# Kernel optimization log

Measured on AMD Instinct MI355X. Metric: run time of the kernel, lower is better.

The kernel has to match this reference:

```python
import jax, jax.numpy as jnp
import numpy as np

N_HEADS = 4
N_HIDDEN = 64  # out_features // n_heads
NEG_SLOPE = 0.2


def setup_inputs() -> dict:
    key = jax.random.key(0)
    k1, k2, k3, k4, k5 = jax.random.split(key, 5)
    B, N, F_IN, F_OUT = 1, 4096, 128, 256
    h = jax.random.normal(k1, (B, N, F_IN), dtype=jnp.float32)
    adj_mat = jax.random.uniform(k2, (N, N, 1), dtype=jnp.float32)
    W_proj = jax.random.normal(k3, (F_IN, N_HEADS * N_HIDDEN), dtype=jnp.float32) / np.sqrt(F_IN)
    W_proj_attn = jax.random.normal(k4, (F_IN, N_HEADS * N_HIDDEN // 2), dtype=jnp.float32) / np.sqrt(F_IN)
    w_attn = jax.random.normal(k5, (N_HIDDEN,), dtype=jnp.float32) / np.sqrt(N_HIDDEN)
    return {"h": h, "adj_mat": adj_mat, "W_proj": W_proj, "W_proj_attn": W_proj_attn, "w_attn": w_attn}


def reference(h, adj_mat, W_proj, W_proj_attn, w_attn):
    B, N, _ = h.shape
    H, D = N_HEADS, N_HIDDEN
    half = D // 2
    # value projection: (B, N, H, D)
    g = (h @ W_proj).reshape(B, N, H, D)
    # attention-feature projection: (B, N, H, D//2)
    ga = (h @ W_proj_attn).reshape(B, N, H, half)
    # attn(cat([ga_i, ga_j])) decomposes linearly: e_ij = <w_l, ga_i> + <w_r, ga_j>
    # (identical math to the torch repeat/cat/Linear, without the NxNxD tensor)
    el = jnp.einsum('bnhk,k->bnh', ga, w_attn[:half])   # dest node i term
    er = jnp.einsum('bnhk,k->bnh', ga, w_attn[half:])   # source node j term
    e = jax.nn.leaky_relu(el[:, :, None, :] + er[:, None, :, :], NEG_SLOPE)  # (B, N, N, H)
    mask = adj_mat >= 0.5  # (N, N, 1) broadcasts over (B, N, N, H)
    e = jnp.where(mask, e, -jnp.inf)
    a = jax.nn.softmax(e, axis=2)  # softmax over source nodes j
    # dropout is identity in eval mode
    out = jnp.einsum('bijh,bjhf->bihf', a, g)  # (B, N, H, D)
    return out.reshape(B, N, H * D)  # is_concat=True
```

## Files before the change

### kernel.cpp

```cpp
#include <hip/hip_runtime.h>
#include <hip/hip_bf16.h>

typedef __bf16 bf16_t;
typedef __bf16 bf16x4 __attribute__((ext_vector_type(4)));
typedef __bf16 bf16x8 __attribute__((ext_vector_type(8)));
typedef float floatx4 __attribute__((ext_vector_type(4)));

#define N_NODES 4096
#define F_IN 128
#define NUM_HEADS 4
#define D_HID 64
#define F_OUT 256
#define NEG_SLOPE 0.2f

__global__ __launch_bounds__(384) void proj_kernel(
    const float* __restrict__ hmat, const float* __restrict__ Wp,
    const float* __restrict__ Wa, const float* __restrict__ wattn,
    bf16_t* __restrict__ GB, float* __restrict__ el, float* __restrict__ er)
{
    __shared__ float hl[4][F_IN];
    const int t = threadIdx.x;
    const int j0 = blockIdx.x * 4;

    if (t < 128) {
        const int jl = t >> 5, m0 = (t & 31) * 4;
        *reinterpret_cast<float4*>(&hl[jl][m0]) =
            *reinterpret_cast<const float4*>(&hmat[(size_t)(j0 + jl) * F_IN + m0]);
    }
    __syncthreads();

    float acc[4] = {0.f, 0.f, 0.f, 0.f};

    const float* wptr;
    int stride;
    if (t < 256) { wptr = Wp + t;         stride = 256; }
    else         { wptr = Wa + (t - 256); stride = 128; }

    for (int m = 0; m < F_IN; m += 4) {
        const float w0 = wptr[(size_t)(m + 0) * stride];
        const float w1 = wptr[(size_t)(m + 1) * stride];
        const float w2 = wptr[(size_t)(m + 2) * stride];
        const float w3 = wptr[(size_t)(m + 3) * stride];
#pragma unroll
        for (int jl = 0; jl < 4; ++jl) {
            const float4 hv = *reinterpret_cast<const float4*>(&hl[jl][m]);
            acc[jl] = fmaf(hv.w, w3, fmaf(hv.z, w2, fmaf(hv.y, w1, fmaf(hv.x, w0, acc[jl]))));
        }
    }

    if (t < 256) {
        const int h = t >> 6, f = t & 63;
        bf16x4 o;
#pragma unroll
        for (int q = 0; q < 4; ++q) o[q] = (bf16_t)acc[q];
        const size_t base = ((((size_t)h * 128 + (j0 >> 5)) * 4 + (f >> 4)) * 64
                             + (f & 15) + 16 * ((j0 >> 3) & 3)) * 8 + (j0 & 7);
        *reinterpret_cast<bf16x4*>(&GB[base]) = o;
    } else {
        const int ta = t - 256;
        const int ha = ta >> 5, k = ta & 31;
        const float wl = wattn[k], wr = wattn[32 + k];
#pragma unroll
        for (int jl = 0; jl < 4; ++jl) {
            float vl = acc[jl] * wl;
            float vr = acc[jl] * wr;
#pragma unroll
            for (int s = 16; s >= 1; s >>= 1) {
                vl += __shfl_xor(vl, s, 64);
                vr += __shfl_xor(vr, s, 64);
            }
            if (k == 0) {
                el[ha * N_NODES + j0 + jl] = vl;
                er[ha * N_NODES + j0 + jl] = vr;
            }
        }
    }
}

__global__ __launch_bounds__(1024) void attn_kernel(
    const float* __restrict__ adj, const bf16_t* __restrict__ GB,
    const float* __restrict__ el, const float* __restrict__ er,
    float* __restrict__ numout, float* __restrict__ den_g,
    int njc, int ntiles)
{
    __shared__ bf16_t P_s[NUM_HEADS * 64 * 64];
    __shared__ bf16_t GB_s[32 * 512];

    const int tid = threadIdx.x;
    const int i0  = blockIdx.x * 64;
    const int jc  = blockIdx.y;
    const int jT0 = jc * ntiles * 64;

    const int pi   = tid >> 4;
    const int pj4  = (tid & 15) << 2;
    const int glog = pj4 >> 3;
    const int goff = pj4 & 7;
    const int psw  = ((glog ^ (pi & 7)) << 3) + goff;

    const int wave = tid >> 6;
    const int hh   = wave >> 2;
    const int mt   = wave & 3;
    const int lane = tid & 63;
    const int m    = lane & 15;
    const int quad = lane >> 4;

    float elr[NUM_HEADS];
#pragma unroll
    for (int h = 0; h < NUM_HEADS; ++h) elr[h] = el[h * N_NODES + i0 + pi];

    const float* adjp = adj + (size_t)(i0 + pi) * N_NODES + pj4;

    const int s0 = wave * 2, s1 = s0 + 1;
    const int s0h = (s0 >> 2) & 3, s0f = s0 & 3, s0j = s0 >> 4;
    const int s1h = (s1 >> 2) & 3, s1f = s1 & 3, s1j = s1 >> 4;

    floatx4 acc0 = {0.f, 0.f, 0.f, 0.f};
    floatx4 acc1 = acc0, acc2 = acc0, acc3 = acc0, accd = acc0;
    bf16x8 ones;
#pragma unroll
    for (int q = 0; q < 8; ++q) ones[q] = (bf16_t)1.0f;

    int jb32 = jT0 >> 5;
    float4 adjv = *reinterpret_cast<const float4*>(adjp + jT0);
    float4 gbv0 = *reinterpret_cast<const float4*>(GB + ((size_t)(s0h * 128 + jb32 + s0j) * 4 + s0f) * 512 + lane * 8);
    float4 gbv1 = *reinterpret_cast<const float4*>(GB + ((size_t)(s1h * 128 + jb32 + s1j) * 4 + s1f) * 512 + lane * 8);

    for (int k = 0; k < ntiles; ++k) {
        const int jT = jT0 + k * 64;
        *reinterpret_cast<float4*>(&GB_s[s0 * 512 + lane * 8]) = gbv0;
        *reinterpret_cast<float4*>(&GB_s[s1 * 512 + lane * 8]) = gbv1;
        float4 adjn, gbn0, gbn1;
        if (k + 1 < ntiles) {
            const int jbn = (jT + 64) >> 5;
            adjn = *reinterpret_cast<const float4*>(adjp + jT + 64);
            gbn0 = *reinterpret_cast<const float4*>(GB + ((size_t)(s0h * 128 + jbn + s0j) * 4 + s0f) * 512 + lane * 8);
            gbn1 = *reinterpret_cast<const float4*>(GB + ((size_t)(s1h * 128 + jbn + s1j) * 4 + s1f) * 512 + lane * 8);
        }
        const bool k0 = adjv.x >= 0.5f, k1 = adjv.y >= 0.5f,
                   k2 = adjv.z >= 0.5f, k3 = adjv.w >= 0.5f;
#pragma unroll
        for (int h = 0; h < NUM_HEADS; ++h) {
            const float4 ev = *reinterpret_cast<const float4*>(er + h * N_NODES + jT + pj4);
            float e0 = elr[h] + ev.x, e1 = elr[h] + ev.y,
                  e2 = elr[h] + ev.z, e3 = elr[h] + ev.w;
            e0 = fmaxf(e0, NEG_SLOPE * e0);
            e1 = fmaxf(e1, NEG_SLOPE * e1);
            e2 = fmaxf(e2, NEG_SLOPE * e2);
            e3 = fmaxf(e3, NEG_SLOPE * e3);
            bf16x4 pv;
            pv[0] = (bf16_t)(k0 ? __expf(e0) : 0.f);
            pv[1] = (bf16_t)(k1 ? __expf(e1) : 0.f);
            pv[2] = (bf16_t)(k2 ? __expf(e2) : 0.f);
            pv[3] = (bf16_t)(k3 ? __expf(e3) : 0.f);
            *reinterpret_cast<bf16x4*>(&P_s[(h * 64 + pi) * 64 + psw]) = pv;
        }
        __syncthreads();
#pragma unroll
        for (int kt = 0; kt < 2; ++kt) {
            const int gphys = (((kt * 4 + quad) ^ (m & 7)) << 3);
            const bf16x8 af = *reinterpret_cast<const bf16x8*>(
                &P_s[(hh * 64 + mt * 16 + m) * 64 + gphys]);
            accd = __builtin_amdgcn_mfma_f32_16x16x32_bf16(af, ones, accd, 0, 0, 0);
            const int bb = (kt * 16 + hh * 4) * 512 + lane * 8;
            const bf16x8 b0 = *reinterpret_cast<const bf16x8*>(&GB_s[bb]);
            const bf16x8 b1 = *reinterpret_cast<const bf16x8*>(&GB_s[bb + 512]);
            const bf16x8 b2 = *reinterpret_cast<const bf16x8*>(&GB_s[bb + 1024]);
            const bf16x8 b3 = *reinterpret_cast<const bf16x8*>(&GB_s[bb + 1536]);
            acc0 = __builtin_amdgcn_mfma_f32_16x16x32_bf16(af, b0, acc0, 0, 0, 0);
            acc1 = __builtin_amdgcn_mfma_f32_16x16x32_bf16(af, b1, acc1, 0, 0, 0);
            acc2 = __builtin_amdgcn_mfma_f32_16x16x32_bf16(af, b2, acc2, 0, 0, 0);
            acc3 = __builtin_amdgcn_mfma_f32_16x16x32_bf16(af, b3, acc3, 0, 0, 0);
        }
        if (k + 1 < ntiles) { adjv = adjn; gbv0 = gbn0; gbv1 = gbn1; }
        __syncthreads();
    }

    const int ibase = i0 + mt * 16 + quad * 4;
    if (njc == 1) {
#pragma unroll
        for (int r = 0; r < 4; ++r) {
            const float rd = 1.0f / accd[r];
            float* dst = numout + (size_t)(ibase + r) * F_OUT + hh * D_HID + m;
            dst[0]  = acc0[r] * rd;
            dst[16] = acc1[r] * rd;
            dst[32] = acc2[r] * rd;
            dst[48] = acc3[r] * rd;
        }
    } else {
        float* nrow = numout + (size_t)jc * ((size_t)N_NODES * F_OUT);
#pragma unroll
        for (int r = 0; r < 4; ++r) {
            float* dst = nrow + (size_t)(ibase + r) * F_OUT + hh * D_HID + m;
            dst[0]  = acc0[r];
            dst[16] = acc1[r];
            dst[32] = acc2[r];
            dst[48] = acc3[r];
        }
        if (m == 0) {
#pragma unroll
            for (int r = 0; r < 4; ++r)
                den_g[((size_t)jc * N_NODES + ibase + r) * NUM_HEADS + hh] = accd[r];
        }
    }
}

__global__ __launch_bounds__(256) void reduce_kernel(
    const float* __restrict__ num, const float* __restrict__ den,
    float* __restrict__ out, int njc)
{
    const int idx = blockIdx.x * 256 + threadIdx.x;
    const int i  = idx >> 8;
    const int c  = idx & 255;
    const int hh = c >> 6;
    float n = 0.f, d = 0.f;
    for (int jc = 0; jc < njc; ++jc) {
        n += num[(size_t)jc * ((size_t)N_NODES * F_OUT) + idx];
        d += den[((size_t)jc * N_NODES + i) * NUM_HEADS + hh];
    }
    out[idx] = n / d;
}

extern "C" void kernel_launch(void* const* d_in, const int* in_sizes, int n_in,
                              void* d_out, int out_size, void* d_ws, size_t ws_size,
                              hipStream_t stream)
{
    const float* hmat = (const float*)d_in[0];
    const float* adj  = (const float*)d_in[1];
    const float* Wp   = (const float*)d_in[2];
    const float* Wa   = (const float*)d_in[3];
    const float* watt = (const float*)d_in[4];
    float* out = (float*)d_out;

    char* ws = (char*)d_ws;
    bf16_t* GB = (bf16_t*)ws;
    float*  el = (float*)(ws + (2ull << 20));
    float*  er = (float*)(ws + (2ull << 20) + (64ull << 10));
    const size_t baseoff = (2ull << 20) + (128ull << 10);

    const size_t num_bytes = (size_t)N_NODES * F_OUT * 4;
    const size_t den_bytes = (size_t)N_NODES * NUM_HEADS * 4;
    const int njc = (ws_size >= baseoff + 4 * (num_bytes + den_bytes)) ? 4 : 2;

    float* num = (float*)(ws + baseoff);
    float* den = (float*)(ws + baseoff + (size_t)njc * num_bytes);

    proj_kernel<<<1024, 384, 0, stream>>>(hmat, Wp, Wa, watt, GB, el, er);
    attn_kernel<<<dim3(64, njc), 1024, 0, stream>>>(adj, GB, el, er, num, den,
                                                    njc, (N_NODES / njc) / 64);
    reduce_kernel<<<(N_NODES * F_OUT) / 256, 256, 0, stream>>>(num, den, out, njc);
}
```

Baseline: 156.1 us.

## Factor exp of leaky-relu into precomputed per-node exponentials and halve row tile

Rewrites exp(leaky_relu(el_i+er_j)) as a selected product of per-node exponentials: exp(er) and exp(0.2*er) are precomputed in the projection kernel, exp(el) and exp(0.2*el) per row, and the branch is chosen by comparing against exp(-el). This removes the per-element transcendental from the attention inner loop, replacing it with a compare, a multiply and an extra global load. The attention block is also shrunk to 32 rows and 512 threads, doubling the grid, with each wave staging four GB slices instead of two. Risks are overflow or precision loss in the unnormalized exponent products and a doubled total read of adj-independent GB tiles.

```diff
diff --git a/kernel.cpp b/kernel.cpp
--- a/kernel.cpp
+++ b/kernel.cpp
@@ -16,7 +16,8 @@
 __global__ __launch_bounds__(384) void proj_kernel(
     const float* __restrict__ hmat, const float* __restrict__ Wp,
     const float* __restrict__ Wa, const float* __restrict__ wattn,
-    bf16_t* __restrict__ GB, float* __restrict__ el, float* __restrict__ er)
+    bf16_t* __restrict__ GB, float* __restrict__ el,
+    float* __restrict__ E1r, float* __restrict__ E2r)
 {
     __shared__ float hl[4][F_IN];
     const int t = threadIdx.x;
@@ -70,24 +71,26 @@
                 vr += __shfl_xor(vr, s, 64);
             }
             if (k == 0) {
-                el[ha * N_NODES + j0 + jl] = vl;
-                er[ha * N_NODES + j0 + jl] = vr;
+                el[ha * N_NODES + j0 + jl]  = vl;
+                E1r[ha * N_NODES + j0 + jl] = __expf(vr);
+                E2r[ha * N_NODES + j0 + jl] = __expf(NEG_SLOPE * vr);
             }
         }
     }
 }
 
-__global__ __launch_bounds__(1024) void attn_kernel(
+__global__ __launch_bounds__(512) void attn_kernel(
     const float* __restrict__ adj, const bf16_t* __restrict__ GB,
-    const float* __restrict__ el, const float* __restrict__ er,
+    const float* __restrict__ el, const float* __restrict__ E1r,
+    const float* __restrict__ E2r,
     float* __restrict__ numout, float* __restrict__ den_g,
     int njc, int ntiles)
 {
-    __shared__ bf16_t P_s[NUM_HEADS * 64 * 64];
+    __shared__ bf16_t P_s[NUM_HEADS * 32 * 64];
     __shared__ bf16_t GB_s[32 * 512];
 
     const int tid = threadIdx.x;
-    const int i0  = blockIdx.x * 64;
+    const int i0  = blockIdx.x * 32;
     const int jc  = blockIdx.y;
     const int jT0 = jc * ntiles * 64;
 
@@ -98,21 +101,29 @@
     const int psw  = ((glog ^ (pi & 7)) << 3) + goff;
 
     const int wave = tid >> 6;
-    const int hh   = wave >> 2;
-    const int mt   = wave & 3;
+    const int hh   = wave >> 1;
+    const int mt   = wave & 1;
     const int lane = tid & 63;
     const int m    = lane & 15;
     const int quad = lane >> 4;
 
-    float elr[NUM_HEADS];
-#pragma unroll
-    for (int h = 0; h < NUM_HEADS; ++h) elr[h] = el[h * N_NODES + i0 + pi];
+    float E1i[NUM_HEADS], E2i[NUM_HEADS], Ti[NUM_HEADS];
+#pragma unroll
+    for (int h = 0; h < NUM_HEADS; ++h) {
+        const float e = el[h * N_NODES + i0 + pi];
+        E1i[h] = __expf(e);
+        E2i[h] = __expf(NEG_SLOPE * e);
+        Ti[h]  = __expf(-e);
+    }
 
     const float* adjp = adj + (size_t)(i0 + pi) * N_NODES + pj4;
 
-    const int s0 = wave * 2, s1 = s0 + 1;
-    const int s0h = (s0 >> 2) & 3, s0f = s0 & 3, s0j = s0 >> 4;
-    const int s1h = (s1 >> 2) & 3, s1f = s1 & 3, s1j = s1 >> 4;
+    int sh[4], sf[4], sj[4];
+#pragma unroll
+    for (int ss = 0; ss < 4; ++ss) {
+        const int s = wave * 4 + ss;
+        sh[ss] = (s >> 2) & 3; sf[ss] = s & 3; sj[ss] = s >> 4;
+    }
 
     floatx4 acc0 = {0.f, 0.f, 0.f, 0.f};
     floatx4 acc1 = acc0, acc2 = acc0, acc3 = acc0, accd = acc0;
@@ -120,46 +131,53 @@
 #pragma unroll
     for (int q = 0; q < 8; ++q) ones[q] = (bf16_t)1.0f;
 
-    int jb32 = jT0 >> 5;
+    const int jb32 = jT0 >> 5;
     float4 adjv = *reinterpret_cast<const float4*>(adjp + jT0);
-    float4 gbv0 = *reinterpret_cast<const float4*>(GB + ((size_t)(s0h * 128 + jb32 + s0j) * 4 + s0f) * 512 + lane * 8);
-    float4 gbv1 = *reinterpret_cast<const float4*>(GB + ((size_t)(s1h * 128 + jb32 + s1j) * 4 + s1f) * 512 + lane * 8);
+    float4 gbv[4];
+#pragma unroll
+    for (int ss = 0; ss < 4; ++ss)
+        gbv[ss] = *reinterpret_cast<const float4*>(
+            GB + ((size_t)(sh[ss] * 128 + jb32 + sj[ss]) * 4 + sf[ss]) * 512 + lane * 8);
 
     for (int k = 0; k < ntiles; ++k) {
         const int jT = jT0 + k * 64;
-        *reinterpret_cast<float4*>(&GB_s[s0 * 512 + lane * 8]) = gbv0;
-        *reinterpret_cast<float4*>(&GB_s[s1 * 512 + lane * 8]) = gbv1;
-        float4 adjn, gbn0, gbn1;
+#pragma unroll
+        for (int ss = 0; ss < 4; ++ss)
+            *reinterpret_cast<float4*>(&GB_s[(wave * 4 + ss) * 512 + lane * 8]) = gbv[ss];
+
+        float4 adjn, gbn[4];
         if (k + 1 < ntiles) {
             const int jbn = (jT + 64) >> 5;
             adjn = *reinterpret_cast<const float4*>(adjp + jT + 64);
-            gbn0 = *reinterpret_cast<const float4*>(GB + ((size_t)(s0h * 128 + jbn + s0j) * 4 + s0f) * 512 + lane * 8);
-            gbn1 = *reinterpret_cast<const float4*>(GB + ((size_t)(s1h * 128 + jbn + s1j) * 4 + s1f) * 512 + lane * 8);
-        }
+#pragma unroll
+            for (int ss = 0; ss < 4; ++ss)
+                gbn[ss] = *reinterpret_cast<const float4*>(
+                    GB + ((size_t)(sh[ss] * 128 + jbn + sj[ss]) * 4 + sf[ss]) * 512 + lane * 8);
+        }
+
         const bool k0 = adjv.x >= 0.5f, k1 = adjv.y >= 0.5f,
                    k2 = adjv.z >= 0.5f, k3 = adjv.w >= 0.5f;
 #pragma unroll
         for (int h = 0; h < NUM_HEADS; ++h) {
-            const float4 ev = *reinterpret_cast<const float4*>(er + h * N_NODES + jT + pj4);
-            float e0 = elr[h] + ev.x, e1 = elr[h] + ev.y,
-                  e2 = elr[h] + ev.z, e3 = elr[h] + ev.w;
-            e0 = fmaxf(e0, NEG_SLOPE * e0);
-            e1 = fmaxf(e1, NEG_SLOPE * e1);
-            e2 = fmaxf(e2, NEG_SLOPE * e2);
-            e3 = fmaxf(e3, NEG_SLOPE * e3);
+            const float4 a1 = *reinterpret_cast<const float4*>(E1r + h * N_NODES + jT + pj4);
+            const float4 a2 = *reinterpret_cast<const float4*>(E2r + h * N_NODES + jT + pj4);
+            const float p0 = (a1.x > Ti[h]) ? E1i[h] * a1.x : E2i[h] * a2.x;
+            const float p1 = (a1.y > Ti[h]) ? E1i[h] * a1.y : E2i[h] * a2.y;
+            const float p2 = (a1.z > Ti[h]) ? E1i[h] * a1.z : E2i[h] * a2.z;
+            const float p3 = (a1.w > Ti[h]) ? E1i[h] * a1.w : E2i[h] * a2.w;
             bf16x4 pv;
-            pv[0] = (bf16_t)(k0 ? __expf(e0) : 0.f);
-            pv[1] = (bf16_t)(k1 ? __expf(e1) : 0.f);
-            pv[2] = (bf16_t)(k2 ? __expf(e2) : 0.f);
-            pv[3] = (bf16_t)(k3 ? __expf(e3) : 0.f);
-            *reinterpret_cast<bf16x4*>(&P_s[(h * 64 + pi) * 64 + psw]) = pv;
+            pv[0] = (bf16_t)(k0 ? p0 : 0.f);
+            pv[1] = (bf16_t)(k1 ? p1 : 0.f);
+            pv[2] = (bf16_t)(k2 ? p2 : 0.f);
+            pv[3] = (bf16_t)(k3 ? p3 : 0.f);
+            *reinterpret_cast<bf16x4*>(&P_s[(h * 32 + pi) * 64 + psw]) = pv;
         }
         __syncthreads();
 #pragma unroll
         for (int kt = 0; kt < 2; ++kt) {
             const int gphys = (((kt * 4 + quad) ^ (m & 7)) << 3);
             const bf16x8 af = *reinterpret_cast<const bf16x8*>(
-                &P_s[(hh * 64 + mt * 16 + m) * 64 + gphys]);
+                &P_s[(hh * 32 + mt * 16 + m) * 64 + gphys]);
             accd = __builtin_amdgcn_mfma_f32_16x16x32_bf16(af, ones, accd, 0, 0, 0);
             const int bb = (kt * 16 + hh * 4) * 512 + lane * 8;
             const bf16x8 b0 = *reinterpret_cast<const bf16x8*>(&GB_s[bb]);
@@ -171,7 +189,11 @@
             acc2 = __builtin_amdgcn_mfma_f32_16x16x32_bf16(af, b2, acc2, 0, 0, 0);
             acc3 = __builtin_amdgcn_mfma_f32_16x16x32_bf16(af, b3, acc3, 0, 0, 0);
         }
-        if (k + 1 < ntiles) { adjv = adjn; gbv0 = gbn0; gbv1 = gbn1; }
+        if (k + 1 < ntiles) {
+            adjv = adjn;
+#pragma unroll
+            for (int ss = 0; ss < 4; ++ss) gbv[ss] = gbn[ss];
+        }
         __syncthreads();
     }
 
@@ -232,10 +254,11 @@
     float* out = (float*)d_out;
 
     char* ws = (char*)d_ws;
-    bf16_t* GB = (bf16_t*)ws;
-    float*  el = (float*)(ws + (2ull << 20));
-    float*  er = (float*)(ws + (2ull << 20) + (64ull << 10));
-    const size_t baseoff = (2ull << 20) + (128ull << 10);
+    bf16_t* GB  = (bf16_t*)ws;
+    float*  el  = (float*)(ws + (2ull << 20));
+    float*  E1r = (float*)(ws + (2ull << 20) + (64ull << 10));
+    float*  E2r = (float*)(ws + (2ull << 20) + (128ull << 10));
+    const size_t baseoff = (2ull << 20) + (192ull << 10);
 
     const size_t num_bytes = (size_t)N_NODES * F_OUT * 4;
     const size_t den_bytes = (size_t)N_NODES * NUM_HEADS * 4;
@@ -244,8 +267,8 @@
     float* num = (float*)(ws + baseoff);
     float* den = (float*)(ws + baseoff + (size_t)njc * num_bytes);
 
-    proj_kernel<<<1024, 384, 0, stream>>>(hmat, Wp, Wa, watt, GB, el, er);
-    attn_kernel<<<dim3(64, njc), 1024, 0, stream>>>(adj, GB, el, er, num, den,
-                                                    njc, (N_NODES / njc) / 64);
+    proj_kernel<<<1024, 384, 0, stream>>>(hmat, Wp, Wa, watt, GB, el, E1r, E2r);
+    attn_kernel<<<dim3(128, njc), 512, 0, stream>>>(adj, GB, el, E1r, E2r,
+                                                    num, den, njc, (N_NODES / njc) / 64);
     reduce_kernel<<<(N_NODES * F_OUT) / 256, 256, 0, stream>>>(num, den, out, njc);
 }
```

After: 334.7 us. 114% more time.
